# Kernel optimization log

Hardware: AMD Instinct MI355X
Metric: run time of the kernel (lower is better)

## Reference

```python
import jax, jax.numpy as jnp
import numpy as np

B, NPQ, NPV, NSL, K, ED, H = 64, 1024, 256, 1, 128, 16, 8
DK = K // H  # per-head dim (k_dim = v_dim = emb_dim // num_heads)
ETYPES = [("PQ","PQ"),("PQ","PV"),("PQ","Slack"),("PV","PQ"),("PV","PV"),("PV","Slack"),("Slack","PQ"),("Slack","PV")]
ECOUNTS = [262144, 131072, 4096, 131072, 65536, 2048, 4096, 2048]
NN = {"PQ": B*NPQ, "PV": B*NPV, "Slack": B*NSL}
LN_EPS = 1e-5


def setup_inputs() -> dict:
    ks = iter(jax.random.split(jax.random.key(0), 64))
    inp = {}
    for name, n in [("x_PQ", NN["PQ"]), ("x_PV", NN["PV"]), ("x_Slack", NN["Slack"])]:
        inp[name] = jax.random.normal(next(ks), (n, K), jnp.float32)
    for t, ((s, d), E) in enumerate(zip(ETYPES, ECOUNTS)):
        src = jax.random.randint(next(ks), (E,), 0, NN[s])
        dst = jax.random.randint(next(ks), (E,), 0, NN[d])
        inp[f"ei_{t}"] = jnp.stack([src, dst]).astype(jnp.int32)
        inp[f"ea_{t}"] = jax.random.normal(next(ks), (E, ED), jnp.float32)
    sc = 1.0 / np.sqrt(K)
    shapes = {"Wk": (2,8,K,K), "bk": (2,8,K), "Wq": (2,8,K,K), "bq": (2,8,K),
              "Wv": (2,8,K,K), "bv": (2,8,K), "Ws": (2,8,K,K), "bconv": (2,8,K),
              "We": (2,8,ED,K), "be": (2,8,K), "Wgt": (K,K), "bgt": (K,),
              "Wq1": (K,K), "Wk2": (K,K), "Wv2": (K,K), "Wo": (K,K), "bo": (K,)}
    for name, sh in shapes.items():
        inp[name] = jax.random.normal(next(ks), sh, jnp.float32) * sc
    inp["ln_g"] = jnp.ones((K,), jnp.float32)
    inp["ln_b"] = jnp.zeros((K,), jnp.float32)
    return inp


def _cross_attention(x1, x2, Wq1, Wk2, Wv2, Wo, bo):
    # x1: [B, N1, K] queries; x2: [B, N2, K] keys/values
    Bq, N1, _ = x1.shape
    N2 = x2.shape[1]
    q = (x1 @ Wq1).reshape(Bq, N1, H, DK)
    k = (x2 @ Wk2).reshape(Bq, N2, H, DK)
    v = (x2 @ Wv2).reshape(Bq, N2, H, DK)
    attn = jnp.einsum("bnhd,bmhd->bhnm", q, k) / np.sqrt(DK).astype(np.float32)
    attn = jax.nn.softmax(attn, axis=-1)
    out = jnp.einsum("bhnm,bmhd->bnhd", attn, v).reshape(Bq, N1, H * DK)
    return out @ Wo + bo


def _forward(x_PQ, x_PV, x_Slack, ei, ea,
             Wk, bk, Wq, bq, Wv, bv, Ws, bconv, We, be,
             Wgt, bgt, Wq1, Wk2, Wv2, Wo, bo, ln_g, ln_b):
    x = {"PQ": x_PQ, "PV": x_PV, "Slack": x_Slack}
    # global feature from input node features
    gf = jnp.concatenate([x_PQ.reshape(B, NPQ, K),
                          x_PV.reshape(B, NPV, K),
                          x_Slack.reshape(B, NSL, K)], axis=1)
    gf = gf @ Wgt + bgt
    gnode = jnp.concatenate([gf.mean(axis=1, keepdims=True),
                             gf.max(axis=1, keepdims=True)], axis=1)  # [B, 2, K]
    # 2 HeteroConv layers of ResGatedGraphConv, aggr='sum' over edge types
    for l in range(2):
        new = {t: jnp.zeros((NN[t], K), x_PQ.dtype) for t in ("PQ", "PV", "Slack")}
        for t, (s, d) in enumerate(ETYPES):
            xs, xd = x[s], x[d]
            k_ = xd @ Wk[l, t] + bk[l, t]   # lin_key on dst
            q_ = xs @ Wq[l, t] + bq[l, t]   # lin_query on src
            v_ = xs @ Wv[l, t] + bv[l, t]   # lin_value on src
            e_ = ea[t] @ We[l, t] + be[l, t]  # lin_edge
            si, di = ei[t][0], ei[t][1]
            gate = jax.nn.sigmoid(k_[di] + q_[si] + e_)  # [E, K]
            agg = jax.ops.segment_sum(gate * v_[si], di, num_segments=NN[d])
            new[d] = new[d] + agg + xd @ Ws[l, t] + bconv[l, t]
        x = {t: jax.nn.relu(v) for t, v in new.items()}
    # cross-attention vs. global mean/max nodes, residual, layernorm (PQ, PV only)
    res = {}
    for key2, N1 in (("PQ", NPQ), ("PV", NPV)):
        x1 = x[key2].reshape(B, N1, K)
        ca = _cross_attention(x1, gnode, Wq1, Wk2, Wv2, Wo, bo).reshape(B * N1, K)
        h = x[key2] + ca
        mu = h.mean(axis=-1, keepdims=True)
        var = ((h - mu) ** 2).mean(axis=-1, keepdims=True)
        res[key2] = (h - mu) * jax.lax.rsqrt(var + LN_EPS) * ln_g + ln_b
    return res["PQ"], res["PV"], x["Slack"]


def reference(x_PQ, x_PV, x_Slack,
              ei_0, ei_1, ei_2, ei_3, ei_4, ei_5, ei_6, ei_7,
              ea_0, ea_1, ea_2, ea_3, ea_4, ea_5, ea_6, ea_7,
              Wk, bk, Wq, bq, Wv, bv, Ws, bconv, We, be,
              Wgt, bgt, Wq1, Wk2, Wv2, Wo, bo, ln_g, ln_b):
    ei = [ei_0, ei_1, ei_2, ei_3, ei_4, ei_5, ei_6, ei_7]
    ea = [ea_0, ea_1, ea_2, ea_3, ea_4, ea_5, ea_6, ea_7]
    return _forward(x_PQ, x_PV, x_Slack, ei, ea,
                    Wk, bk, Wq, bq, Wv, bv, Ws, bconv, We, be,
                    Wgt, bgt, Wq1, Wk2, Wv2, Wo, bo, ln_g, ln_b)
```

## Files before the change

kernel.cpp:

```cpp
#include <hip/hip_runtime.h>
#include <hip/hip_bf16.h>
#include <math.h>

#define N_PQ 65536
#define N_PV 16384
#define N_SL 64

typedef __attribute__((ext_vector_type(8))) short s16x8;
typedef __attribute__((ext_vector_type(4))) float f32x4;

__device__ __forceinline__ ushort f2bf(float f) {
    union { float f; unsigned u; } x; x.f = f;
    unsigned r = x.u + 0x7fff + ((x.u >> 16) & 1);
    return (ushort)(r >> 16);
}
__device__ __forceinline__ float bf2f(ushort u) {
    union { unsigned u; float f; } x; x.u = ((unsigned)u) << 16;
    return x.f;
}

template<int OUT_BF16, int MLOOP>
__global__ __launch_bounds__(256) void gemm_mfma(
    const ushort* __restrict__ A, const ushort* __restrict__ Bt,
    const float* __restrict__ bias, void* __restrict__ Cv, int M, int N)
{
    __shared__ ushort As[128 * 128];
    const int tid = threadIdx.x;
    const int n0 = blockIdx.y * 128;
    const int lane = tid & 63, wave = tid >> 6;
    const int wr = wave >> 1, wc = wave & 1;
    const int lrow = lane & 15, lk = lane >> 4;

    #pragma unroll 1
    for (int it = 0; it < MLOOP; ++it) {
        const int m0 = (blockIdx.x * MLOOP + it) * 128;
        if (m0 >= M) break;
        if (it) __syncthreads();

        #pragma unroll
        for (int p = 0; p < 8; ++p) {
            int c = p * 256 + tid;
            int row = c >> 4, c16 = c & 15;
            int gr = m0 + row;
            int4 v = make_int4(0, 0, 0, 0);
            if (gr < M) v = *(const int4*)(A + (size_t)gr * 128 + c16 * 8);
            *(int4*)(As + row * 128 + (c16 ^ (row & 7)) * 8) = v;
        }
        __syncthreads();

        f32x4 acc[4][4];
        #pragma unroll
        for (int mi = 0; mi < 4; ++mi)
            #pragma unroll
            for (int ni = 0; ni < 4; ++ni) acc[mi][ni] = (f32x4){0.f, 0.f, 0.f, 0.f};

        #pragma unroll
        for (int kk = 0; kk < 4; ++kk) {
            s16x8 a[4], b[4];
            #pragma unroll
            for (int mi = 0; mi < 4; ++mi) {
                int row = wr * 64 + mi * 16 + lrow;
                int c16 = (lk + kk * 4) ^ (row & 7);
                a[mi] = *(const s16x8*)(As + row * 128 + c16 * 8);
            }
            #pragma unroll
            for (int ni = 0; ni < 4; ++ni) {
                int n = n0 + wc * 64 + ni * 16 + lrow;
                b[ni] = *(const s16x8*)(Bt + (size_t)n * 128 + kk * 32 + lk * 8);
            }
            #pragma unroll
            for (int mi = 0; mi < 4; ++mi)
                #pragma unroll
                for (int ni = 0; ni < 4; ++ni)
                    acc[mi][ni] = __builtin_amdgcn_mfma_f32_16x16x32_bf16(
                        a[mi], b[ni], acc[mi][ni], 0, 0, 0);
        }

        if (OUT_BF16) {
            __syncthreads();
            ushort* Cl = As;
            #pragma unroll
            for (int mi = 0; mi < 4; ++mi)
                #pragma unroll
                for (int ni = 0; ni < 4; ++ni)
                    #pragma unroll
                    for (int r = 0; r < 4; ++r) {
                        int row = wr * 64 + mi * 16 + (lane >> 4) * 4 + r;
                        int col = wc * 64 + ni * 16 + (lane & 15);
                        float v = acc[mi][ni][r] + (bias ? bias[n0 + col] : 0.f);
                        Cl[row * 128 + (((col >> 3) ^ (row & 7)) << 3) + (col & 7)] = f2bf(v);
                    }
            __syncthreads();
            ushort* C = (ushort*)Cv;
            #pragma unroll
            for (int p = 0; p < 8; ++p) {
                int c = p * 256 + tid;
                int row = c >> 4, c16 = c & 15;
                int gr = m0 + row;
                if (gr < M)
                    *(int4*)(C + (size_t)gr * N + n0 + c16 * 8) =
                        *(const int4*)(As + row * 128 + (c16 ^ (row & 7)) * 8);
            }
        } else {
            float* C = (float*)Cv;
            #pragma unroll
            for (int mi = 0; mi < 4; ++mi)
                #pragma unroll
                for (int ni = 0; ni < 4; ++ni)
                    #pragma unroll
                    for (int r = 0; r < 4; ++r) {
                        int row = m0 + wr * 64 + mi * 16 + (lane >> 4) * 4 + r;
                        int col = n0 + wc * 64 + ni * 16 + (lane & 15);
                        if (row < M)
                            C[(size_t)row * N + col] =
                                acc[mi][ni][r] + (bias ? bias[col] : 0.f);
                    }
        }
    }
}

__global__ void prep_mats(
    const float* __restrict__ Wk, const float* __restrict__ Wq,
    const float* __restrict__ Wv, const float* __restrict__ Ws,
    const float* __restrict__ Wgt, const float* __restrict__ Wq1,
    const float* __restrict__ Wk2, const float* __restrict__ Wv2,
    const float* __restrict__ Wo,
    ushort* __restrict__ panels, ushort* __restrict__ wssum,
    ushort* __restrict__ finalw)
{
    const int m = blockIdx.x >> 6;
    const int e = (blockIdx.x & 63) * 256 + threadIdx.x;
    const int nl = e >> 7, k = e & 127;
    const int dstlist[3][3] = {{0,3,6},{1,4,7},{2,5,-1}};
    const int srclist[3][3] = {{0,1,2},{3,4,5},{6,7,-1}};
    const int nkg[3] = {3,3,2};
    const int gofs[3] = {0,1280,2560};

    if (m < 52) {
        int l = m / 26, r = m % 26;
        int g, slot;
        if (r < 10)      { g = 0; slot = r; }
        else if (r < 20) { g = 1; slot = r - 10; }
        else             { g = 2; slot = r - 20; }
        int nk = nkg[g];
        float val; int col;
        if (slot < nk) {
            int t = dstlist[g][slot];
            val = Wk[(size_t)(l * 8 + t) * 16384 + k * 128 + nl];
            col = slot * 128 + nl;
        } else if (slot < 2 * nk) {
            int s = slot - nk; int t = srclist[g][s];
            val = Wq[(size_t)(l * 8 + t) * 16384 + k * 128 + nl];
            col = nk * 128 + s * 256 + ((nl >> 1) << 2) + (nl & 1);
        } else if (slot < 3 * nk) {
            int s = slot - 2 * nk; int t = srclist[g][s];
            val = Wv[(size_t)(l * 8 + t) * 16384 + k * 128 + nl];
            col = nk * 128 + s * 256 + ((nl >> 1) << 2) + 2 + (nl & 1);
        } else {
            float s = 0.f;
            #pragma unroll
            for (int i = 0; i < 3; ++i) {
                int t = dstlist[g][i];
                if (t >= 0) s += Ws[(size_t)(l * 8 + t) * 16384 + k * 128 + nl];
            }
            val = s; col = 1152 + nl;
        }
        panels[((size_t)l * 3328 + gofs[g] + col) * 128 + k] = f2bf(val);
    } else if (m < 54) {
        int l = m - 52;
        float s = Ws[(size_t)(l * 8 + 2) * 16384 + k * 128 + nl]
                + Ws[(size_t)(l * 8 + 5) * 16384 + k * 128 + nl];
        wssum[(size_t)l * 16384 + nl * 128 + k] = f2bf(s);
    } else {
        const float* fsrc[5] = {Wgt, Wq1, Wk2, Wv2, Wo};
        int idx = m - 54;
        finalw[(size_t)idx * 16384 + nl * 128 + k] = f2bf(fsrc[idx][k * 128 + nl]);
    }
}

__global__ void prep_bias(
    const float* __restrict__ bk, const float* __restrict__ bq,
    const float* __restrict__ bv, const float* __restrict__ bconv,
    float* __restrict__ bias_cat, float* __restrict__ bcsum)
{
    const int l = blockIdx.x / 3, g = blockIdx.x % 3;
    const int dstlist[3][3] = {{0,3,6},{1,4,7},{2,5,-1}};
    const int srclist[3][3] = {{0,1,2},{3,4,5},{6,7,-1}};
    const int nkg[3] = {3,3,2};
    const int gofs[3] = {0,1280,2560};
    const int nslots = (g < 2) ? 10 : 6;
    int nk = nkg[g];
    for (int idx = threadIdx.x; idx < nslots * 128; idx += 256) {
        int slot = idx >> 7, nl = idx & 127;
        float val; int col;
        if (slot < nk) {
            int t = dstlist[g][slot];
            val = bk[(l * 8 + t) * 128 + nl];
            col = slot * 128 + nl;
        } else if (slot < 2 * nk) {
            int s = slot - nk; int t = srclist[g][s];
            val = bq[(l * 8 + t) * 128 + nl];
            col = nk * 128 + s * 256 + ((nl >> 1) << 2) + (nl & 1);
        } else if (slot < 3 * nk) {
            int s = slot - 2 * nk; int t = srclist[g][s];
            val = bv[(l * 8 + t) * 128 + nl];
            col = nk * 128 + s * 256 + ((nl >> 1) << 2) + 2 + (nl & 1);
        } else {
            float s = 0.f;
            #pragma unroll
            for (int i = 0; i < 3; ++i) {
                int t = dstlist[g][i];
                if (t >= 0) s += bconv[(l * 8 + t) * 128 + nl];
            }
            val = s; col = 1152 + nl;
        }
        bias_cat[l * 3328 + gofs[g] + col] = val;
    }
    if (g == 2 && threadIdx.x < 128) {
        bcsum[l * 128 + threadIdx.x] =
            bconv[(l * 8 + 2) * 128 + threadIdx.x] + bconv[(l * 8 + 5) * 128 + threadIdx.x];
    }
}

struct HArgs {
    const int* ei[6];
    int E[6];
    int base[6];
    int cum[7];
};

__global__ void hist_kernel(HArgs A, int* __restrict__ bins)
{
    int g = blockIdx.x * 256 + threadIdx.x;
    if (g >= A.cum[6]) return;
    int t = 0;
    #pragma unroll
    for (int i = 0; i < 5; ++i) t += (g >= A.cum[i + 1]);
    int e = g - A.cum[t];
    int dst = A.ei[t][A.E[t] + e];
    atomicAdd(&bins[A.base[t] + dst], 1);
}

__global__ __launch_bounds__(256) void scan_a(
    const int* __restrict__ bins, int* __restrict__ offs, int* __restrict__ bsum)
{
    __shared__ int s[256];
    const int b = blockIdx.x, t = threadIdx.x;
    int v = bins[b * 256 + t];
    s[t] = v; __syncthreads();
    #pragma unroll
    for (int off = 1; off < 256; off <<= 1) {
        int x = (t >= off) ? s[t - off] : 0;
        __syncthreads();
        s[t] += x;
        __syncthreads();
    }
    offs[b * 256 + t] = s[t] - v;
    if (t == 255) bsum[b] = s[255];
}

__global__ __launch_bounds__(1024) void scan_b(
    const int* __restrict__ bsum, int* __restrict__ carry)
{
    __shared__ int s[1024];
    const int t = threadIdx.x;
    int v = bsum[t];
    s[t] = v; __syncthreads();
    for (int off = 1; off < 1024; off <<= 1) {
        int x = (t >= off) ? s[t - off] : 0;
        __syncthreads();
        s[t] += x;
        __syncthreads();
    }
    carry[t] = s[t] - v;
}

__global__ void scan_c(int* __restrict__ offs, const int* __restrict__ carry,
                       int* __restrict__ cursor)
{
    const int b = blockIdx.x, t = threadIdx.x;
    int v = offs[b * 256 + t] + carry[b];
    offs[b * 256 + t] = v;
    cursor[b * 256 + t] = v;
}

__global__ void scatter_kernel(HArgs A, int* __restrict__ cursor,
                               int* __restrict__ lsrc, int* __restrict__ leid)
{
    int g = blockIdx.x * 256 + threadIdx.x;
    if (g >= A.cum[6]) return;
    int t = 0;
    #pragma unroll
    for (int i = 0; i < 5; ++i) t += (g >= A.cum[i + 1]);
    int e = g - A.cum[t];
    int src = A.ei[t][e];
    int dst = A.ei[t][A.E[t] + e];
    int pos = atomicAdd(&cursor[A.base[t] + dst], 1);
    lsrc[pos] = src;
    leid[pos] = e;
}

struct GTA {
    int base, kcol, qvcol, lds;
    const ushort* Ys;
    const float* ea;
    const float* We;
    const float* be;
};
struct GArgs {
    GTA t[3];
    const int* offs;
    const int* lsrc;
    const int* leid;
    ushort* xbg;
    const ushort* Yg;
    int ldg, wscol;
};

__global__ __launch_bounds__(256) void gather_kernel(GArgs A)
{
    const int wave = threadIdx.x >> 6, lane = threadIdx.x & 63;
    const int d = blockIdx.x * 4 + wave;
    const int j0 = lane * 2;

    ushort2 w2 = *(const ushort2*)(A.Yg + (size_t)d * A.ldg + A.wscol + j0);
    float a0 = bf2f(w2.x), a1 = bf2f(w2.y);

    #pragma unroll
    for (int i = 0; i < 3; ++i) {
        const GTA T = A.t[i];
        int start = __builtin_amdgcn_readfirstlane(A.offs[T.base + d]);
        int end   = __builtin_amdgcn_readfirstlane(A.offs[T.base + d + 1]);
        if (start == end) continue;

        ushort2 kk = *(const ushort2*)(A.Yg + (size_t)d * A.ldg + T.kcol + j0);
        float k0 = bf2f(kk.x), k1 = bf2f(kk.y);
        float we0[16], we1[16];
        #pragma unroll
        for (int r = 0; r < 16; ++r) {
            float2 wv = *(const float2*)(T.We + r * 128 + j0);
            we0[r] = wv.x; we1[r] = wv.y;
        }
        float2 be2 = *(const float2*)(T.be + j0);

        int eB = (start + 1 < end) ? start + 1 : start;
        int siA  = __builtin_amdgcn_readfirstlane(A.lsrc[start]);
        int eidA = __builtin_amdgcn_readfirstlane(A.leid[start]);
        uint2 qvA = *(const uint2*)(T.Ys + (size_t)siA * T.lds + T.qvcol + lane * 4);
        float4 aA0 = *(const float4*)(T.ea + (size_t)eidA * 16);
        float4 aA1 = *(const float4*)(T.ea + (size_t)eidA * 16 + 4);
        float4 aA2 = *(const float4*)(T.ea + (size_t)eidA * 16 + 8);
        float4 aA3 = *(const float4*)(T.ea + (size_t)eidA * 16 + 12);
        int siB  = __builtin_amdgcn_readfirstlane(A.lsrc[eB]);
        int eidB = __builtin_amdgcn_readfirstlane(A.leid[eB]);
        uint2 qvB = *(const uint2*)(T.Ys + (size_t)siB * T.lds + T.qvcol + lane * 4);
        float4 aB0 = *(const float4*)(T.ea + (size_t)eidB * 16);
        float4 aB1 = *(const float4*)(T.ea + (size_t)eidB * 16 + 4);
        float4 aB2 = *(const float4*)(T.ea + (size_t)eidB * 16 + 8);
        float4 aB3 = *(const float4*)(T.ea + (size_t)eidB * 16 + 12);

        #define COMPUTE(QV, C0, C1, C2, C3) { \
            float e0 = be2.x, e1 = be2.y; \
            e0 += (C0).x*we0[0] + (C0).y*we0[1] + (C0).z*we0[2] + (C0).w*we0[3] \
                + (C1).x*we0[4] + (C1).y*we0[5] + (C1).z*we0[6] + (C1).w*we0[7] \
                + (C2).x*we0[8] + (C2).y*we0[9] + (C2).z*we0[10] + (C2).w*we0[11] \
                + (C3).x*we0[12] + (C3).y*we0[13] + (C3).z*we0[14] + (C3).w*we0[15]; \
            e1 += (C0).x*we1[0] + (C0).y*we1[1] + (C0).z*we1[2] + (C0).w*we1[3] \
                + (C1).x*we1[4] + (C1).y*we1[5] + (C1).z*we1[6] + (C1).w*we1[7] \
                + (C2).x*we1[8] + (C2).y*we1[9] + (C2).z*we1[10] + (C2).w*we1[11] \
                + (C3).x*we1[12] + (C3).y*we1[13] + (C3).z*we1[14] + (C3).w*we1[15]; \
            float q0 = bf2f((ushort)((QV).x & 0xffff)), q1 = bf2f((ushort)((QV).x >> 16)); \
            float v0 = bf2f((ushort)((QV).y & 0xffff)), v1 = bf2f((ushort)((QV).y >> 16)); \
            float g0 = 1.f / (1.f + __expf(-(k0 + q0 + e0))); \
            float g1 = 1.f / (1.f + __expf(-(k1 + q1 + e1))); \
            a0 = fmaf(g0, v0, a0); \
            a1 = fmaf(g1, v1, a1); }

        for (int e = start; e < end; e += 2) {
            uint2 qc = qvA;
            float4 c0 = aA0, c1 = aA1, c2 = aA2, c3 = aA3;
            int nxA = (e + 2 < end) ? e + 2 : e;
            siA  = __builtin_amdgcn_readfirstlane(A.lsrc[nxA]);
            eidA = __builtin_amdgcn_readfirstlane(A.leid[nxA]);
            qvA = *(const uint2*)(T.Ys + (size_t)siA * T.lds + T.qvcol + lane * 4);
            aA0 = *(const float4*)(T.ea + (size_t)eidA * 16);
            aA1 = *(const float4*)(T.ea + (size_t)eidA * 16 + 4);
            aA2 = *(const float4*)(T.ea + (size_t)eidA * 16 + 8);
            aA3 = *(const float4*)(T.ea + (size_t)eidA * 16 + 12);
            COMPUTE(qc, c0, c1, c2, c3)

            if (e + 1 < end) {
                uint2 qc2 = qvB;
                float4 d0 = aB0, d1 = aB1, d2 = aB2, d3 = aB3;
                int nxB = (e + 3 < end) ? e + 3 : e;
                siB  = __builtin_amdgcn_readfirstlane(A.lsrc[nxB]);
                eidB = __builtin_amdgcn_readfirstlane(A.leid[nxB]);
                qvB = *(const uint2*)(T.Ys + (size_t)siB * T.lds + T.qvcol + lane * 4);
                aB0 = *(const float4*)(T.ea + (size_t)eidB * 16);
                aB1 = *(const float4*)(T.ea + (size_t)eidB * 16 + 4);
                aB2 = *(const float4*)(T.ea + (size_t)eidB * 16 + 8);
                aB3 = *(const float4*)(T.ea + (size_t)eidB * 16 + 12);
                COMPUTE(qc2, d0, d1, d2, d3)
            }
        }
        #undef COMPUTE
    }
    ushort2 o; o.x = f2bf(fmaxf(a0, 0.f)); o.y = f2bf(fmaxf(a1, 0.f));
    *(ushort2*)(A.xbg + (size_t)d * 128 + j0) = o;
}

__global__ __launch_bounds__(256) void edge_slack(
    const int* __restrict__ ei, const float* __restrict__ ea,
    const float* __restrict__ We, const float* __restrict__ be,
    const ushort* __restrict__ Yk, int ldk,
    const ushort* __restrict__ Yqv, int ldq,
    float* __restrict__ nd, int E)
{
    const int e = blockIdx.x * 2 + (threadIdx.x >> 7);
    if (e >= E) return;
    const int j = threadIdx.x & 127;
    const int si = ei[e];
    const int di = ei[E + e];

    float ej = be[j];
    #pragma unroll
    for (int r = 0; r < 16; ++r)
        ej += ea[(size_t)e * 16 + r] * We[r * 128 + j];

    float kv = bf2f(Yk[(size_t)di * ldk + j]);
    float qv = bf2f(Yqv[(size_t)si * ldq + ((j >> 1) << 2) + (j & 1)]);
    float vv = bf2f(Yqv[(size_t)si * ldq + ((j >> 1) << 2) + 2 + (j & 1)]);
    float g  = 1.f / (1.f + __expf(-(kv + qv + ej)));
    atomicAdd(&nd[(size_t)di * 128 + j], g * vv);
}

__global__ void f2b_kernel(const float* __restrict__ a, ushort* __restrict__ o, int n)
{
    int i = (blockIdx.x * 256 + threadIdx.x) * 4;
    if (i < n) {
        float4 v = *(const float4*)(a + i);
        ushort4 u; u.x = f2bf(v.x); u.y = f2bf(v.y); u.z = f2bf(v.z); u.w = f2bf(v.w);
        *(ushort4*)(o + i) = u;
    }
}
__global__ void relu_b_kernel(const float* __restrict__ a, ushort* __restrict__ o, int n)
{
    int i = (blockIdx.x * 256 + threadIdx.x) * 4;
    if (i < n) {
        float4 v = *(const float4*)(a + i);
        ushort4 u;
        u.x = f2bf(fmaxf(v.x, 0.f)); u.y = f2bf(fmaxf(v.y, 0.f));
        u.z = f2bf(fmaxf(v.z, 0.f)); u.w = f2bf(fmaxf(v.w, 0.f));
        *(ushort4*)(o + i) = u;
    }
}
__global__ void b2f_kernel(const ushort* __restrict__ a, float* __restrict__ o, int n)
{
    int i = blockIdx.x * 256 + threadIdx.x;
    if (i < n) o[i] = bf2f(a[i]);
}

__global__ void pool1(const ushort* __restrict__ gf, float* __restrict__ pbuf)
{
    const int b = blockIdx.x >> 4, c = blockIdx.x & 15;
    const int j = threadIdx.x;
    float s = 0.f, m = -INFINITY;
    const ushort* pq = gf + (size_t)(b * 1024 + c * 64) * 128;
    for (int i = 0; i < 64; ++i) { float v = bf2f(pq[i * 128 + j]); s += v; m = fmaxf(m, v); }
    const ushort* pv = gf + (size_t)(N_PQ + b * 256 + c * 16) * 128;
    for (int i = 0; i < 16; ++i) { float v = bf2f(pv[i * 128 + j]); s += v; m = fmaxf(m, v); }
    if (c == 0) { float v = bf2f(gf[(size_t)(N_PQ + N_PV + b) * 128 + j]); s += v; m = fmaxf(m, v); }
    pbuf[(size_t)blockIdx.x * 256 + j] = s;
    pbuf[(size_t)blockIdx.x * 256 + 128 + j] = m;
}
__global__ void pool2(const float* __restrict__ pbuf, float* __restrict__ gnode)
{
    const int b = blockIdx.x, j = threadIdx.x;
    float s = 0.f, m = -INFINITY;
    for (int c = 0; c < 16; ++c) {
        s += pbuf[(size_t)(b * 16 + c) * 256 + j];
        m = fmaxf(m, pbuf[(size_t)(b * 16 + c) * 256 + 128 + j]);
    }
    gnode[(size_t)(b * 2) * 128 + j]     = s * (1.f / 1281.f);
    gnode[(size_t)(b * 2 + 1) * 128 + j] = m;
}

__global__ __launch_bounds__(256) void attn_kernel(
    const ushort* __restrict__ q, const float* __restrict__ k2,
    const float* __restrict__ v2, ushort* __restrict__ ao, int shift, int Ntot)
{
    const int n = blockIdx.x * 2 + (threadIdx.x >> 7);
    if (n >= Ntot) return;
    const int j = threadIdx.x & 127;
    const int b = n >> shift;
    const int h16 = j & ~15;

    const ushort* qn = q + (size_t)n * 128 + h16;
    const float* k0 = k2 + (size_t)(b * 2) * 128 + h16;
    const float* k1 = k2 + (size_t)(b * 2 + 1) * 128 + h16;
    float s0 = 0.f, s1 = 0.f;
    #pragma unroll
    for (int d = 0; d < 16; ++d) {
        float qq = bf2f(qn[d]); s0 += qq * k0[d]; s1 += qq * k1[d];
    }
    s0 *= 0.25f; s1 *= 0.25f;
    float m  = fmaxf(s0, s1);
    float a0 = __expf(s0 - m), a1 = __expf(s1 - m);
    float inv = 1.f / (a0 + a1);
    ao[(size_t)n * 128 + j] = f2bf(
        (a0 * v2[(size_t)(b * 2) * 128 + j] + a1 * v2[(size_t)(b * 2 + 1) * 128 + j]) * inv);
}

__global__ __launch_bounds__(256) void ln_kernel(
    const ushort* __restrict__ x, const ushort* __restrict__ ca,
    const float* __restrict__ g, const float* __restrict__ bb,
    float* __restrict__ out, int N)
{
    const int n = blockIdx.x * 4 + (threadIdx.x >> 6);
    if (n >= N) return;
    const int l = threadIdx.x & 63;
    const size_t base = (size_t)n * 128;
    float h0 = bf2f(x[base + l * 2])     + bf2f(ca[base + l * 2]);
    float h1 = bf2f(x[base + l * 2 + 1]) + bf2f(ca[base + l * 2 + 1]);
    float s  = h0 + h1;
    float ss = h0 * h0 + h1 * h1;
    #pragma unroll
    for (int o = 32; o; o >>= 1) { s += __shfl_xor(s, o); ss += __shfl_xor(ss, o); }
    float mu  = s * (1.f / 128.f);
    float var = ss * (1.f / 128.f) - mu * mu;
    float rs  = rsqrtf(var + 1e-5f);
    out[base + l * 2]     = (h0 - mu) * rs * g[l * 2]     + bb[l * 2];
    out[base + l * 2 + 1] = (h1 - mu) * rs * g[l * 2 + 1] + bb[l * 2 + 1];
}

extern "C" void kernel_launch(void* const* d_in, const int* in_sizes, int n_in,
                              void* d_out, int out_size, void* d_ws, size_t ws_size,
                              hipStream_t stream)
{
    const float* xin[3] = {(const float*)d_in[0], (const float*)d_in[1], (const float*)d_in[2]};
    const int NNs[3] = {N_PQ, N_PV, N_SL};
    const int ncol[3] = {1280, 1280, 768};
    const int gofs[3] = {0, 1280, 2560};

    const int*   ei[8];
    const float* ea[8];
    int          Ecnt[8];
    for (int t = 0; t < 8; ++t) {
        ei[t]   = (const int*)d_in[3 + 2 * t];
        ea[t]   = (const float*)d_in[4 + 2 * t];
        Ecnt[t] = in_sizes[3 + 2 * t] / 2;
    }
    const float* Wk    = (const float*)d_in[19];
    const float* bk    = (const float*)d_in[20];
    const float* Wq    = (const float*)d_in[21];
    const float* bq    = (const float*)d_in[22];
    const float* Wv    = (const float*)d_in[23];
    const float* bv    = (const float*)d_in[24];
    const float* Ws    = (const float*)d_in[25];
    const float* bconv = (const float*)d_in[26];
    const float* We    = (const float*)d_in[27];
    const float* be    = (const float*)d_in[28];
    const float* Wgt   = (const float*)d_in[29];
    const float* bgt   = (const float*)d_in[30];
    const float* Wq1   = (const float*)d_in[31];
    const float* Wk2   = (const float*)d_in[32];
    const float* Wv2   = (const float*)d_in[33];
    const float* Wo    = (const float*)d_in[34];
    const float* bo    = (const float*)d_in[35];
    const float* ln_g  = (const float*)d_in[36];
    const float* ln_b  = (const float*)d_in[37];

    char* w = (char*)d_ws;
    ushort* Y[3];
    Y[0] = (ushort*)w; w += (size_t)N_PQ * 1280 * 2;
    Y[1] = (ushort*)w; w += (size_t)N_PV * 1280 * 2;
    Y[2] = (ushort*)w; w += (size_t)N_SL * 768 * 2;
    ushort* xb[3];
    xb[0] = (ushort*)w; w += (size_t)N_PQ * 128 * 2;
    xb[1] = (ushort*)w; w += (size_t)N_PV * 128 * 2;
    xb[2] = (ushort*)w; w += (size_t)N_SL * 128 * 2;
    ushort* panels = (ushort*)w; w += (size_t)2 * 3328 * 128 * 2;
    ushort* wssum  = (ushort*)w; w += (size_t)2 * 16384 * 2;
    ushort* finalw = (ushort*)w; w += (size_t)5 * 16384 * 2;
    float* bias_cat = (float*)w; w += 6656 * 4;
    float* bcsum    = (float*)w; w += 256 * 4;
    float* gnode    = (float*)w; w += 16384 * 4;
    ushort* gnodeb  = (ushort*)w; w += 16384 * 2;
    float* k2       = (float*)w; w += 16384 * 4;
    float* v2       = (float*)w; w += 16384 * 4;
    float* pbuf     = (float*)w; w += 1024 * 256 * 4;
    const int NBINS = 262144;
    int* bins   = (int*)w; w += (size_t)NBINS * 4;
    int* offs   = (int*)w; w += (size_t)NBINS * 4;
    int* cursor = (int*)w; w += (size_t)NBINS * 4;
    int* bsum   = (int*)w; w += 1024 * 4;
    int* carry  = (int*)w; w += 1024 * 4;
    int* lsrc   = (int*)w; w += (size_t)600064 * 4;
    int* leid   = (int*)w; w += (size_t)600064 * 4;
    ushort* gf    = Y[0];
    ushort* qb    = Y[0];
    ushort* ao    = Y[0] + (size_t)81920 * 128;
    ushort* cbufb = Y[0] + (size_t)2 * 81920 * 128;
    float* outp = (float*)d_out;
    float* nw2 = outp + (size_t)(N_PQ + N_PV) * 128;

    const ushort* Wgt_t = finalw;
    const ushort* Wq1_t = finalw + 16384;
    const ushort* Wk2_t = finalw + 32768;
    const ushort* Wv2_t = finalw + 49152;
    const ushort* Wo_t  = finalw + 65536;

    auto gemm_b = [&](const ushort* A, const ushort* Bt, const float* bias,
                      ushort* C, int M, int N) {
        int mt = (M + 127) / 128;
        int nblk = mt * (N / 128);
        if (nblk >= 4096 && mt % 4 == 0)
            gemm_mfma<1, 4><<<dim3(mt / 4, N / 128), 256, 0, stream>>>(A, Bt, bias, C, M, N);
        else
            gemm_mfma<1, 1><<<dim3(mt, N / 128), 256, 0, stream>>>(A, Bt, bias, C, M, N);
    };
    auto gemm_f = [&](const ushort* A, const ushort* Bt, const float* bias,
                      float* C, int M, int N) {
        gemm_mfma<0, 1><<<dim3((M + 127) / 128, N / 128), 256, 0, stream>>>(
            A, Bt, bias, C, M, N);
    };

    prep_mats<<<59 * 64, 256, 0, stream>>>(Wk, Wq, Wv, Ws, Wgt, Wq1, Wk2, Wv2, Wo,
                                           panels, wssum, finalw);
    prep_bias<<<6, 256, 0, stream>>>(bk, bq, bv, bconv, bias_cat, bcsum);
    for (int g = 0; g < 3; ++g) {
        int n = NNs[g] * 128;
        f2b_kernel<<<dim3((n / 4 + 255) / 256), 256, 0, stream>>>(xin[g], xb[g], n);
    }

    const int csr_t[6]    = {0, 3, 6, 1, 4, 7};
    const int csr_base[6] = {0, 65536, 131072, 196608, 212992, 229376};
    HArgs ha;
    {
        int c = 0;
        for (int i = 0; i < 6; ++i) {
            int t = csr_t[i];
            ha.ei[i] = ei[t]; ha.E[i] = Ecnt[t]; ha.base[i] = csr_base[i];
            ha.cum[i] = c; c += Ecnt[t];
        }
        ha.cum[6] = c;
    }
    hipMemsetAsync(bins, 0, (size_t)NBINS * 4, stream);
    hist_kernel<<<dim3((ha.cum[6] + 255) / 256), 256, 0, stream>>>(ha, bins);
    scan_a<<<1024, 256, 0, stream>>>(bins, offs, bsum);
    scan_b<<<1, 1024, 0, stream>>>(bsum, carry);
    scan_c<<<1024, 256, 0, stream>>>(offs, carry, cursor);
    scatter_kernel<<<dim3((ha.cum[6] + 255) / 256), 256, 0, stream>>>(ha, cursor, lsrc, leid);

    gemm_b(xb[0], Wgt_t, bgt, gf, N_PQ + N_PV + N_SL, 128);
    pool1<<<1024, 128, 0, stream>>>(gf, pbuf);
    pool2<<<64, 128, 0, stream>>>(pbuf, gnode);
    f2b_kernel<<<dim3(16384 / 4 / 256), 256, 0, stream>>>(gnode, gnodeb, 16384);
    gemm_f(gnodeb, Wk2_t, nullptr, k2, 128, 128);
    gemm_f(gnodeb, Wv2_t, nullptr, v2, 128, 128);

    for (int l = 0; l < 2; ++l) {
        for (int g = 0; g < 3; ++g)
            gemm_b(xb[g], panels + ((size_t)l * 3328 + gofs[g]) * 128,
                   bias_cat + l * 3328 + gofs[g], Y[g], NNs[g], ncol[g]);
        gemm_f(xb[2], wssum + (size_t)l * 16384, bcsum + l * 128, nw2, N_SL, 128);

        for (int g = 0; g < 2; ++g) {
            GArgs ga;
            for (int i = 0; i < 3; ++i) {
                int t = csr_t[g * 3 + i], off = l * 8 + t;
                int sgrp = (i == 2) ? 2 : i;
                ga.t[i].base  = csr_base[g * 3 + i];
                ga.t[i].kcol  = i * 128;
                ga.t[i].lds   = ncol[sgrp];
                ga.t[i].qvcol = ((sgrp == 2) ? 256 : 384) + g * 256;
                ga.t[i].Ys    = Y[sgrp];
                ga.t[i].ea    = ea[t];
                ga.t[i].We    = We + (size_t)off * 2048;
                ga.t[i].be    = be + (size_t)off * 128;
            }
            ga.offs = offs; ga.lsrc = lsrc; ga.leid = leid;
            ga.xbg = xb[g]; ga.Yg = Y[g]; ga.ldg = ncol[g]; ga.wscol = 1152;
            gather_kernel<<<dim3(NNs[g] / 4), 256, 0, stream>>>(ga);
        }

        {
            int off2 = l * 8 + 2;
            edge_slack<<<dim3((Ecnt[2] + 1) / 2), 256, 0, stream>>>(
                ei[2], ea[2], We + (size_t)off2 * 2048, be + (size_t)off2 * 128,
                Y[2] + 0, 768, Y[0] + 896, 1280, nw2, Ecnt[2]);
            int off5 = l * 8 + 5;
            edge_slack<<<dim3((Ecnt[5] + 1) / 2), 256, 0, stream>>>(
                ei[5], ea[5], We + (size_t)off5 * 2048, be + (size_t)off5 * 128,
                Y[2] + 128, 768, Y[1] + 896, 1280, nw2, Ecnt[5]);
        }
        relu_b_kernel<<<dim3(8), 256, 0, stream>>>(nw2, xb[2], N_SL * 128);
    }

    gemm_b(xb[0], Wq1_t, nullptr, qb, N_PQ + N_PV, 128);
    attn_kernel<<<dim3(N_PQ / 2), 256, 0, stream>>>(qb, k2, v2, ao, 10, N_PQ);
    attn_kernel<<<dim3(N_PV / 2), 256, 0, stream>>>(qb + (size_t)N_PQ * 128, k2, v2,
                                                    ao + (size_t)N_PQ * 128, 8, N_PV);
    gemm_b(ao, Wo_t, bo, cbufb, N_PQ + N_PV, 128);
    ln_kernel<<<dim3((N_PQ + N_PV) / 4), 256, 0, stream>>>(xb[0], cbufb, ln_g, ln_b,
                                                           outp, N_PQ + N_PV);
    b2f_kernel<<<dim3((N_SL * 128 + 255) / 256), 256, 0, stream>>>(
        xb[2], outp + (size_t)(N_PQ + N_PV) * 128, N_SL * 128);
}
```

Baseline: 993.6 us.

## Pre-sort edge attributes into CSR order as bf16; drop multi-tile GEMM loop

The scatter kernel now also writes each edge's 16 attributes, converted to bf16, into a buffer laid out in CSR (destination-sorted) order. The gather kernel can then read them sequentially instead of fetching fp32 rows randomly through the edge id. This path is used only when the workspace is large enough, and the edge-id loads are skipped on it. Separately, the GEMM's MLOOP multi-tile persistent loop is removed, so every launch uses one 128-row tile per block. The cost is an extra write pass at scatter time plus bf16 rounding of the edge attributes.

```diff
diff --git a/kernel.cpp b/kernel.cpp
--- a/kernel.cpp
+++ b/kernel.cpp
@@ -19,103 +19,98 @@
     return x.f;
 }
 
-template<int OUT_BF16, int MLOOP>
+template<int OUT_BF16>
 __global__ __launch_bounds__(256) void gemm_mfma(
     const ushort* __restrict__ A, const ushort* __restrict__ Bt,
     const float* __restrict__ bias, void* __restrict__ Cv, int M, int N)
 {
     __shared__ ushort As[128 * 128];
     const int tid = threadIdx.x;
+    const int m0 = blockIdx.x * 128;
     const int n0 = blockIdx.y * 128;
+
+    #pragma unroll
+    for (int p = 0; p < 8; ++p) {
+        int c = p * 256 + tid;
+        int row = c >> 4, c16 = c & 15;
+        int gr = m0 + row;
+        int4 v = make_int4(0, 0, 0, 0);
+        if (gr < M) v = *(const int4*)(A + (size_t)gr * 128 + c16 * 8);
+        *(int4*)(As + row * 128 + (c16 ^ (row & 7)) * 8) = v;
+    }
+    __syncthreads();
+
     const int lane = tid & 63, wave = tid >> 6;
     const int wr = wave >> 1, wc = wave & 1;
     const int lrow = lane & 15, lk = lane >> 4;
 
-    #pragma unroll 1
-    for (int it = 0; it < MLOOP; ++it) {
-        const int m0 = (blockIdx.x * MLOOP + it) * 128;
-        if (m0 >= M) break;
-        if (it) __syncthreads();
-
+    f32x4 acc[4][4];
+    #pragma unroll
+    for (int mi = 0; mi < 4; ++mi)
+        #pragma unroll
+        for (int ni = 0; ni < 4; ++ni) acc[mi][ni] = (f32x4){0.f, 0.f, 0.f, 0.f};
+
+    #pragma unroll
+    for (int kk = 0; kk < 4; ++kk) {
+        s16x8 a[4], b[4];
+        #pragma unroll
+        for (int mi = 0; mi < 4; ++mi) {
+            int row = wr * 64 + mi * 16 + lrow;
+            int c16 = (lk + kk * 4) ^ (row & 7);
+            a[mi] = *(const s16x8*)(As + row * 128 + c16 * 8);
+        }
+        #pragma unroll
+        for (int ni = 0; ni < 4; ++ni) {
+            int n = n0 + wc * 64 + ni * 16 + lrow;
+            b[ni] = *(const s16x8*)(Bt + (size_t)n * 128 + kk * 32 + lk * 8);
+        }
+        #pragma unroll
+        for (int mi = 0; mi < 4; ++mi)
+            #pragma unroll
+            for (int ni = 0; ni < 4; ++ni)
+                acc[mi][ni] = __builtin_amdgcn_mfma_f32_16x16x32_bf16(
+                    a[mi], b[ni], acc[mi][ni], 0, 0, 0);
+    }
+
+    if (OUT_BF16) {
+        __syncthreads();
+        ushort* Cl = As;
+        #pragma unroll
+        for (int mi = 0; mi < 4; ++mi)
+            #pragma unroll
+            for (int ni = 0; ni < 4; ++ni)
+                #pragma unroll
+                for (int r = 0; r < 4; ++r) {
+                    int row = wr * 64 + mi * 16 + (lane >> 4) * 4 + r;
+                    int col = wc * 64 + ni * 16 + (lane & 15);
+                    float v = acc[mi][ni][r] + (bias ? bias[n0 + col] : 0.f);
+                    Cl[row * 128 + (((col >> 3) ^ (row & 7)) << 3) + (col & 7)] = f2bf(v);
+                }
+        __syncthreads();
+        ushort* C = (ushort*)Cv;
         #pragma unroll
         for (int p = 0; p < 8; ++p) {
             int c = p * 256 + tid;
             int row = c >> 4, c16 = c & 15;
             int gr = m0 + row;
-            int4 v = make_int4(0, 0, 0, 0);
-            if (gr < M) v = *(const int4*)(A + (size_t)gr * 128 + c16 * 8);
-            *(int4*)(As + row * 128 + (c16 ^ (row & 7)) * 8) = v;
-        }
-        __syncthreads();
-
-        f32x4 acc[4][4];
+            if (gr < M)
+                *(int4*)(C + (size_t)gr * N + n0 + c16 * 8) =
+                    *(const int4*)(As + row * 128 + (c16 ^ (row & 7)) * 8);
+        }
+    } else {
+        float* C = (float*)Cv;
         #pragma unroll
         for (int mi = 0; mi < 4; ++mi)
             #pragma unroll
-            for (int ni = 0; ni < 4; ++ni) acc[mi][ni] = (f32x4){0.f, 0.f, 0.f, 0.f};
-
-        #pragma unroll
-        for (int kk = 0; kk < 4; ++kk) {
-            s16x8 a[4], b[4];
-            #pragma unroll
-            for (int mi = 0; mi < 4; ++mi) {
-                int row = wr * 64 + mi * 16 + lrow;
-                int c16 = (lk + kk * 4) ^ (row & 7);
-                a[mi] = *(const s16x8*)(As + row * 128 + c16 * 8);
-            }
-            #pragma unroll
-            for (int ni = 0; ni < 4; ++ni) {
-                int n = n0 + wc * 64 + ni * 16 + lrow;
-                b[ni] = *(const s16x8*)(Bt + (size_t)n * 128 + kk * 32 + lk * 8);
-            }
-            #pragma unroll
-            for (int mi = 0; mi < 4; ++mi)
+            for (int ni = 0; ni < 4; ++ni)
                 #pragma unroll
-                for (int ni = 0; ni < 4; ++ni)
-                    acc[mi][ni] = __builtin_amdgcn_mfma_f32_16x16x32_bf16(
-                        a[mi], b[ni], acc[mi][ni], 0, 0, 0);
-        }
-
-        if (OUT_BF16) {
-            __syncthreads();
-            ushort* Cl = As;
-            #pragma unroll
-            for (int mi = 0; mi < 4; ++mi)
-                #pragma unroll
-                for (int ni = 0; ni < 4; ++ni)
-                    #pragma unroll
-                    for (int r = 0; r < 4; ++r) {
-                        int row = wr * 64 + mi * 16 + (lane >> 4) * 4 + r;
-                        int col = wc * 64 + ni * 16 + (lane & 15);
-                        float v = acc[mi][ni][r] + (bias ? bias[n0 + col] : 0.f);
-                        Cl[row * 128 + (((col >> 3) ^ (row & 7)) << 3) + (col & 7)] = f2bf(v);
-                    }
-            __syncthreads();
-            ushort* C = (ushort*)Cv;
-            #pragma unroll
-            for (int p = 0; p < 8; ++p) {
-                int c = p * 256 + tid;
-                int row = c >> 4, c16 = c & 15;
-                int gr = m0 + row;
-                if (gr < M)
-                    *(int4*)(C + (size_t)gr * N + n0 + c16 * 8) =
-                        *(const int4*)(As + row * 128 + (c16 ^ (row & 7)) * 8);
-            }
-        } else {
-            float* C = (float*)Cv;
-            #pragma unroll
-            for (int mi = 0; mi < 4; ++mi)
-                #pragma unroll
-                for (int ni = 0; ni < 4; ++ni)
-                    #pragma unroll
-                    for (int r = 0; r < 4; ++r) {
-                        int row = m0 + wr * 64 + mi * 16 + (lane >> 4) * 4 + r;
-                        int col = n0 + wc * 64 + ni * 16 + (lane & 15);
-                        if (row < M)
-                            C[(size_t)row * N + col] =
-                                acc[mi][ni][r] + (bias ? bias[col] : 0.f);
-                    }
-        }
+                for (int r = 0; r < 4; ++r) {
+                    int row = m0 + wr * 64 + mi * 16 + (lane >> 4) * 4 + r;
+                    int col = n0 + wc * 64 + ni * 16 + (lane & 15);
+                    if (row < M)
+                        C[(size_t)row * N + col] =
+                            acc[mi][ni][r] + (bias ? bias[col] : 0.f);
+                }
     }
 }
 
@@ -224,6 +219,7 @@
 
 struct HArgs {
     const int* ei[6];
+    const float* eav[6];
     int E[6];
     int base[6];
     int cum[7];
@@ -285,7 +281,8 @@
 }
 
 __global__ void scatter_kernel(HArgs A, int* __restrict__ cursor,
-                               int* __restrict__ lsrc, int* __restrict__ leid)
+                               int* __restrict__ lsrc, int* __restrict__ leid,
+                               ushort* __restrict__ eascat)
 {
     int g = blockIdx.x * 256 + threadIdx.x;
     if (g >= A.cum[6]) return;
@@ -298,6 +295,17 @@
     int pos = atomicAdd(&cursor[A.base[t] + dst], 1);
     lsrc[pos] = src;
     leid[pos] = e;
+    if (eascat) {
+        const float* eap = A.eav[t] + (size_t)e * 16;
+        s16x8 lo, hi;
+        #pragma unroll
+        for (int r = 0; r < 8; ++r) {
+            lo[r] = (short)f2bf(eap[r]);
+            hi[r] = (short)f2bf(eap[r + 8]);
+        }
+        *(s16x8*)(eascat + (size_t)pos * 16) = lo;
+        *(s16x8*)(eascat + (size_t)pos * 16 + 8) = hi;
+    }
 }
 
 struct GTA {
@@ -312,11 +320,13 @@
     const int* offs;
     const int* lsrc;
     const int* leid;
+    const ushort* eascat;
     ushort* xbg;
     const ushort* Yg;
     int ldg, wscol;
 };
 
+template<int SEQEA>
 __global__ __launch_bounds__(256) void gather_kernel(GArgs A)
 {
     const int wave = threadIdx.x >> 6, lane = threadIdx.x & 63;
@@ -343,67 +353,119 @@
         }
         float2 be2 = *(const float2*)(T.be + j0);
 
-        int eB = (start + 1 < end) ? start + 1 : start;
-        int siA  = __builtin_amdgcn_readfirstlane(A.lsrc[start]);
-        int eidA = __builtin_amdgcn_readfirstlane(A.leid[start]);
-        uint2 qvA = *(const uint2*)(T.Ys + (size_t)siA * T.lds + T.qvcol + lane * 4);
-        float4 aA0 = *(const float4*)(T.ea + (size_t)eidA * 16);
-        float4 aA1 = *(const float4*)(T.ea + (size_t)eidA * 16 + 4);
-        float4 aA2 = *(const float4*)(T.ea + (size_t)eidA * 16 + 8);
-        float4 aA3 = *(const float4*)(T.ea + (size_t)eidA * 16 + 12);
-        int siB  = __builtin_amdgcn_readfirstlane(A.lsrc[eB]);
-        int eidB = __builtin_amdgcn_readfirstlane(A.leid[eB]);
-        uint2 qvB = *(const uint2*)(T.Ys + (size_t)siB * T.lds + T.qvcol + lane * 4);
-        float4 aB0 = *(const float4*)(T.ea + (size_t)eidB * 16);
-        float4 aB1 = *(const float4*)(T.ea + (size_t)eidB * 16 + 4);
-        float4 aB2 = *(const float4*)(T.ea + (size_t)eidB * 16 + 8);
-        float4 aB3 = *(const float4*)(T.ea + (size_t)eidB * 16 + 12);
-
-        #define COMPUTE(QV, C0, C1, C2, C3) { \
-            float e0 = be2.x, e1 = be2.y; \
-            e0 += (C0).x*we0[0] + (C0).y*we0[1] + (C0).z*we0[2] + (C0).w*we0[3] \
-                + (C1).x*we0[4] + (C1).y*we0[5] + (C1).z*we0[6] + (C1).w*we0[7] \
-                + (C2).x*we0[8] + (C2).y*we0[9] + (C2).z*we0[10] + (C2).w*we0[11] \
-                + (C3).x*we0[12] + (C3).y*we0[13] + (C3).z*we0[14] + (C3).w*we0[15]; \
-            e1 += (C0).x*we1[0] + (C0).y*we1[1] + (C0).z*we1[2] + (C0).w*we1[3] \
-                + (C1).x*we1[4] + (C1).y*we1[5] + (C1).z*we1[6] + (C1).w*we1[7] \
-                + (C2).x*we1[8] + (C2).y*we1[9] + (C2).z*we1[10] + (C2).w*we1[11] \
-                + (C3).x*we1[12] + (C3).y*we1[13] + (C3).z*we1[14] + (C3).w*we1[15]; \
+        #define FINISH(QV, E0, E1) { \
             float q0 = bf2f((ushort)((QV).x & 0xffff)), q1 = bf2f((ushort)((QV).x >> 16)); \
             float v0 = bf2f((ushort)((QV).y & 0xffff)), v1 = bf2f((ushort)((QV).y >> 16)); \
-            float g0 = 1.f / (1.f + __expf(-(k0 + q0 + e0))); \
-            float g1 = 1.f / (1.f + __expf(-(k1 + q1 + e1))); \
+            float g0 = 1.f / (1.f + __expf(-(k0 + q0 + (E0)))); \
+            float g1 = 1.f / (1.f + __expf(-(k1 + q1 + (E1)))); \
             a0 = fmaf(g0, v0, a0); \
             a1 = fmaf(g1, v1, a1); }
 
-        for (int e = start; e < end; e += 2) {
-            uint2 qc = qvA;
-            float4 c0 = aA0, c1 = aA1, c2 = aA2, c3 = aA3;
-            int nxA = (e + 2 < end) ? e + 2 : e;
-            siA  = __builtin_amdgcn_readfirstlane(A.lsrc[nxA]);
-            eidA = __builtin_amdgcn_readfirstlane(A.leid[nxA]);
-            qvA = *(const uint2*)(T.Ys + (size_t)siA * T.lds + T.qvcol + lane * 4);
-            aA0 = *(const float4*)(T.ea + (size_t)eidA * 16);
-            aA1 = *(const float4*)(T.ea + (size_t)eidA * 16 + 4);
-            aA2 = *(const float4*)(T.ea + (size_t)eidA * 16 + 8);
-            aA3 = *(const float4*)(T.ea + (size_t)eidA * 16 + 12);
-            COMPUTE(qc, c0, c1, c2, c3)
-
-            if (e + 1 < end) {
-                uint2 qc2 = qvB;
-                float4 d0 = aB0, d1 = aB1, d2 = aB2, d3 = aB3;
-                int nxB = (e + 3 < end) ? e + 3 : e;
-                siB  = __builtin_amdgcn_readfirstlane(A.lsrc[nxB]);
-                eidB = __builtin_amdgcn_readfirstlane(A.leid[nxB]);
-                qvB = *(const uint2*)(T.Ys + (size_t)siB * T.lds + T.qvcol + lane * 4);
-                aB0 = *(const float4*)(T.ea + (size_t)eidB * 16);
-                aB1 = *(const float4*)(T.ea + (size_t)eidB * 16 + 4);
-                aB2 = *(const float4*)(T.ea + (size_t)eidB * 16 + 8);
-                aB3 = *(const float4*)(T.ea + (size_t)eidB * 16 + 12);
-                COMPUTE(qc2, d0, d1, d2, d3)
+        if (SEQEA) {
+            int eB = (start + 1 < end) ? start + 1 : start;
+            int siA = __builtin_amdgcn_readfirstlane(A.lsrc[start]);
+            uint2 qvA = *(const uint2*)(T.Ys + (size_t)siA * T.lds + T.qvcol + lane * 4);
+            s16x8 loA = *(const s16x8*)(A.eascat + (size_t)start * 16);
+            s16x8 hiA = *(const s16x8*)(A.eascat + (size_t)start * 16 + 8);
+            int siB = __builtin_amdgcn_readfirstlane(A.lsrc[eB]);
+            uint2 qvB = *(const uint2*)(T.Ys + (size_t)siB * T.lds + T.qvcol + lane * 4);
+            s16x8 loB = *(const s16x8*)(A.eascat + (size_t)eB * 16);
+            s16x8 hiB = *(const s16x8*)(A.eascat + (size_t)eB * 16 + 8);
+
+            #define COMPUTE_SEQ(QV, LO, HI) { \
+                float c[16]; \
+                _Pragma("unroll") \
+                for (int r = 0; r < 8; ++r) { \
+                    c[r]     = bf2f((ushort)(LO)[r]); \
+                    c[r + 8] = bf2f((ushort)(HI)[r]); \
+                } \
+                float e0 = be2.x, e1 = be2.y; \
+                _Pragma("unroll") \
+                for (int r = 0; r < 16; ++r) { \
+                    e0 = fmaf(c[r], we0[r], e0); \
+                    e1 = fmaf(c[r], we1[r], e1); \
+                } \
+                FINISH(QV, e0, e1) }
+
+            for (int e = start; e < end; e += 2) {
+                uint2 qc = qvA; s16x8 cl = loA, ch = hiA;
+                int nxA = (e + 2 < end) ? e + 2 : e;
+                siA = __builtin_amdgcn_readfirstlane(A.lsrc[nxA]);
+                qvA = *(const uint2*)(T.Ys + (size_t)siA * T.lds + T.qvcol + lane * 4);
+                loA = *(const s16x8*)(A.eascat + (size_t)nxA * 16);
+                hiA = *(const s16x8*)(A.eascat + (size_t)nxA * 16 + 8);
+                COMPUTE_SEQ(qc, cl, ch)
+
+                if (e + 1 < end) {
+                    uint2 qc2 = qvB; s16x8 dl = loB, dh = hiB;
+                    int nxB = (e + 3 < end) ? e + 3 : e;
+                    siB = __builtin_amdgcn_readfirstlane(A.lsrc[nxB]);
+                    qvB = *(const uint2*)(T.Ys + (size_t)siB * T.lds + T.qvcol + lane * 4);
+                    loB = *(const s16x8*)(A.eascat + (size_t)nxB * 16);
+                    hiB = *(const s16x8*)(A.eascat + (size_t)nxB * 16 + 8);
+                    COMPUTE_SEQ(qc2, dl, dh)
+                }
             }
-        }
-        #undef COMPUTE
+            #undef COMPUTE_SEQ
+        } else {
+            int eB = (start + 1 < end) ? start + 1 : start;
+            int siA  = __builtin_amdgcn_readfirstlane(A.lsrc[start]);
+            int eidA = __builtin_amdgcn_readfirstlane(A.leid[start]);
+            uint2 qvA = *(const uint2*)(T.Ys + (size_t)siA * T.lds + T.qvcol + lane * 4);
+            float4 aA0 = *(const float4*)(T.ea + (size_t)eidA * 16);
+            float4 aA1 = *(const float4*)(T.ea + (size_t)eidA * 16 + 4);
+            float4 aA2 = *(const float4*)(T.ea + (size_t)eidA * 16 + 8);
+            float4 aA3 = *(const float4*)(T.ea + (size_t)eidA * 16 + 12);
+            int siB  = __builtin_amdgcn_readfirstlane(A.lsrc[eB]);
+            int eidB = __builtin_amdgcn_readfirstlane(A.leid[eB]);
+            uint2 qvB = *(const uint2*)(T.Ys + (size_t)siB * T.lds + T.qvcol + lane * 4);
+            float4 aB0 = *(const float4*)(T.ea + (size_t)eidB * 16);
+            float4 aB1 = *(const float4*)(T.ea + (size_t)eidB * 16 + 4);
+            float4 aB2 = *(const float4*)(T.ea + (size_t)eidB * 16 + 8);
+            float4 aB3 = *(const float4*)(T.ea + (size_t)eidB * 16 + 12);
+
+            #define COMPUTE(QV, C0, C1, C2, C3) { \
+                float e0 = be2.x, e1 = be2.y; \
+                e0 += (C0).x*we0[0] + (C0).y*we0[1] + (C0).z*we0[2] + (C0).w*we0[3] \
+                    + (C1).x*we0[4] + (C1).y*we0[5] + (C1).z*we0[6] + (C1).w*we0[7] \
+                    + (C2).x*we0[8] + (C2).y*we0[9] + (C2).z*we0[10] + (C2).w*we0[11] \
+                    + (C3).x*we0[12] + (C3).y*we0[13] + (C3).z*we0[14] + (C3).w*we0[15]; \
+                e1 += (C0).x*we1[0] + (C0).y*we1[1] + (C0).z*we1[2] + (C0).w*we1[3] \
+                    + (C1).x*we1[4] + (C1).y*we1[5] + (C1).z*we1[6] + (C1).w*we1[7] \
+                    + (C2).x*we1[8] + (C2).y*we1[9] + (C2).z*we1[10] + (C2).w*we1[11] \
+                    + (C3).x*we1[12] + (C3).y*we1[13] + (C3).z*we1[14] + (C3).w*we1[15]; \
+                FINISH(QV, e0, e1) }
+
+            for (int e = start; e < end; e += 2) {
+                uint2 qc = qvA;
+                float4 c0 = aA0, c1 = aA1, c2 = aA2, c3 = aA3;
+                int nxA = (e + 2 < end) ? e + 2 : e;
+                siA  = __builtin_amdgcn_readfirstlane(A.lsrc[nxA]);
+                eidA = __builtin_amdgcn_readfirstlane(A.leid[nxA]);
+                qvA = *(const uint2*)(T.Ys + (size_t)siA * T.lds + T.qvcol + lane * 4);
+                aA0 = *(const float4*)(T.ea + (size_t)eidA * 16);
+                aA1 = *(const float4*)(T.ea + (size_t)eidA * 16 + 4);
+                aA2 = *(const float4*)(T.ea + (size_t)eidA * 16 + 8);
+                aA3 = *(const float4*)(T.ea + (size_t)eidA * 16 + 12);
+                COMPUTE(qc, c0, c1, c2, c3)
+
+                if (e + 1 < end) {
+                    uint2 qc2 = qvB;
+                    float4 d0 = aB0, d1 = aB1, d2 = aB2, d3 = aB3;
+                    int nxB = (e + 3 < end) ? e + 3 : e;
+                    siB  = __builtin_amdgcn_readfirstlane(A.lsrc[nxB]);
+                    eidB = __builtin_amdgcn_readfirstlane(A.leid[nxB]);
+                    qvB = *(const uint2*)(T.Ys + (size_t)siB * T.lds + T.qvcol + lane * 4);
+                    aB0 = *(const float4*)(T.ea + (size_t)eidB * 16);
+                    aB1 = *(const float4*)(T.ea + (size_t)eidB * 16 + 4);
+                    aB2 = *(const float4*)(T.ea + (size_t)eidB * 16 + 8);
+                    aB3 = *(const float4*)(T.ea + (size_t)eidB * 16 + 12);
+                    COMPUTE(qc2, d0, d1, d2, d3)
+                }
+            }
+            #undef COMPUTE
+        }
+        #undef FINISH
     }
     ushort2 o; o.x = f2bf(fmaxf(a0, 0.f)); o.y = f2bf(fmaxf(a1, 0.f));
     *(ushort2*)(A.xbg + (size_t)d * 128 + j0) = o;
@@ -597,6 +659,12 @@
     int* carry  = (int*)w; w += 1024 * 4;
     int* lsrc   = (int*)w; w += (size_t)600064 * 4;
     int* leid   = (int*)w; w += (size_t)600064 * 4;
+    size_t base_bytes = (size_t)(w - (char*)d_ws);
+    size_t eascat_bytes = (size_t)600064 * 16 * 2;
+    ushort* eascat = nullptr;
+    if (base_bytes + eascat_bytes <= ws_size) {
+        eascat = (ushort*)w; w += eascat_bytes;
+    }
     ushort* gf    = Y[0];
     ushort* qb    = Y[0];
     ushort* ao    = Y[0] + (size_t)81920 * 128;
@@ -612,17 +680,11 @@
 
     auto gemm_b = [&](const ushort* A, const ushort* Bt, const float* bias,
                       ushort* C, int M, int N) {
-        int mt = (M + 127) / 128;
-        int nblk = mt * (N / 128);
-        if (nblk >= 4096 && mt % 4 == 0)
-            gemm_mfma<1, 4><<<dim3(mt / 4, N / 128), 256, 0, stream>>>(A, Bt, bias, C, M, N);
-        else
-            gemm_mfma<1, 1><<<dim3(mt, N / 128), 256, 0, stream>>>(A, Bt, bias, C, M, N);
+        gemm_mfma<1><<<dim3((M + 127) / 128, N / 128), 256, 0, stream>>>(A, Bt, bias, C, M, N);
     };
     auto gemm_f = [&](const ushort* A, const ushort* Bt, const float* bias,
                       float* C, int M, int N) {
-        gemm_mfma<0, 1><<<dim3((M + 127) / 128, N / 128), 256, 0, stream>>>(
-            A, Bt, bias, C, M, N);
+        gemm_mfma<0><<<dim3((M + 127) / 128, N / 128), 256, 0, stream>>>(A, Bt, bias, C, M, N);
     };
 
     prep_mats<<<59 * 64, 256, 0, stream>>>(Wk, Wq, Wv, Ws, Wgt, Wq1, Wk2, Wv2, Wo,
@@ -640,7 +702,8 @@
         int c = 0;
         for (int i = 0; i < 6; ++i) {
             int t = csr_t[i];
-            ha.ei[i] = ei[t]; ha.E[i] = Ecnt[t]; ha.base[i] = csr_base[i];
+            ha.ei[i] = ei[t]; ha.eav[i] = ea[t];
+            ha.E[i] = Ecnt[t]; ha.base[i] = csr_base[i];
             ha.cum[i] = c; c += Ecnt[t];
         }
         ha.cum[6] = c;
@@ -650,7 +713,8 @@
     scan_a<<<1024, 256, 0, stream>>>(bins, offs, bsum);
     scan_b<<<1, 1024, 0, stream>>>(bsum, carry);
     scan_c<<<1024, 256, 0, stream>>>(offs, carry, cursor);
-    scatter_kernel<<<dim3((ha.cum[6] + 255) / 256), 256, 0, stream>>>(ha, cursor, lsrc, leid);
+    scatter_kernel<<<dim3((ha.cum[6] + 255) / 256), 256, 0, stream>>>(
+        ha, cursor, lsrc, leid, eascat);
 
     gemm_b(xb[0], Wgt_t, bgt, gf, N_PQ + N_PV + N_SL, 128);
     pool1<<<1024, 128, 0, stream>>>(gf, pbuf);
@@ -679,9 +743,12 @@
                 ga.t[i].We    = We + (size_t)off * 2048;
                 ga.t[i].be    = be + (size_t)off * 128;
             }
-            ga.offs = offs; ga.lsrc = lsrc; ga.leid = leid;
+            ga.offs = offs; ga.lsrc = lsrc; ga.leid = leid; ga.eascat = eascat;
             ga.xbg = xb[g]; ga.Yg = Y[g]; ga.ldg = ncol[g]; ga.wscol = 1152;
-            gather_kernel<<<dim3(NNs[g] / 4), 256, 0, stream>>>(ga);
+            if (eascat)
+                gather_kernel<1><<<dim3(NNs[g] / 4), 256, 0, stream>>>(ga);
+            else
+                gather_kernel<0><<<dim3(NNs[g] / 4), 256, 0, stream>>>(ga);
         }
 
         {
```

New measurement: 882.5 us. 11.2% less time.
